# Optimization experiments

Measured on AMD Instinct MI355X. Metric: run time of the kernel, lower is better.

Reference implementation:

```python
import jax, jax.numpy as jnp
import numpy as np

B, H, S, D = 2, 16, 2048, 64

def setup_inputs() -> dict:
    key = jax.random.key(0)
    kq, kk, kv, km, ks = jax.random.split(key, 5)
    return {
        "query_input": jax.random.normal(kq, (B, H, S, D), dtype=jnp.float32),
        "key_input": jax.random.normal(kk, (B, H, S, D), dtype=jnp.float32),
        "value_input": jax.random.normal(kv, (B, H, S, D), dtype=jnp.float32),
        "query_mask": jnp.ones((B, 1, S, 1), dtype=jnp.float32),
        "key_mask": jax.random.uniform(km, (B, 1, 1, S), dtype=jnp.float32),
        "scale_factor": jax.random.normal(ks, (B, 1, 1, 1), dtype=jnp.float32),
        "dropout": 0,
    }

def reference(query_input, key_input, value_input, query_mask, key_mask, scale_factor, dropout):
    # qk = q @ k^T  -> [B, H, S, S]
    qk = jnp.einsum("bhqd,bhkd->bhqk", query_input, key_input)
    scaled_qk = qk * scale_factor                      # elementwise per-batch scale
    softmax_qk = jax.nn.softmax(scaled_qk, axis=-1)
    masked = softmax_qk * key_mask                     # post-softmax multiplicative mask
    # dropout with p=0 is the identity (deterministic baseline)
    output = jnp.einsum("bhqk,bhkd->bhqd", masked, value_input)
    return output
```

## Files before the change

kernel.cpp:

```cpp
#include <hip/hip_runtime.h>
#include <hip/hip_bf16.h>
#include <stdint.h>

#define BB 2
#define HH 16
#define SS 2048
#define DD 64
constexpr int BH = BB * HH;
constexpr int NT = SS / 64;
constexpr int QB = 16;

typedef _Float16 f16_t;
typedef f16_t f16x8 __attribute__((ext_vector_type(8)));
typedef float f32x4 __attribute__((ext_vector_type(4)));

__device__ __forceinline__ uint32_t pkf16(float a, float b) {
    return __builtin_bit_cast(uint32_t, __builtin_amdgcn_cvt_pkrtz(a, b));
}
__device__ __forceinline__ float fmax3(float a, float b, float c) {
    return fmaxf(fmaxf(a, b), c);
}

__global__ __launch_bounds__(256)
void prepack(const float* __restrict__ Kg, const float* __restrict__ Vg,
             const float* __restrict__ Mg, f16_t* __restrict__ Kp,
             f16_t* __restrict__ Vp)
{
    __shared__ float Vs[64][65];
    const int bh = blockIdx.x % BH;
    const int kt = blockIdx.x / BH;
    const int b  = bh / HH;
    const int t  = threadIdx.x;
    const size_t gbase = (size_t)bh * SS * DD + (size_t)kt * 64 * DD;
    const size_t tbase = ((size_t)bh * NT + kt) * 4096;

    for (int c = t; c < 512; c += 256) {
        const int row = c >> 3, j = c & 7;
        const float* kp = Kg + gbase + (size_t)row * DD + j * 8;
        float4 a = *(const float4*)kp;
        float4 d = *(const float4*)(kp + 4);
        uint4 w = make_uint4(pkf16(a.x, a.y), pkf16(a.z, a.w),
                             pkf16(d.x, d.y), pkf16(d.z, d.w));
        *(uint4*)&Kp[tbase + (size_t)row * 64 + ((j ^ (row & 7)) * 8)] = w;
    }

    for (int c = t; c < 1024; c += 256) {
        const int key = c >> 4, dc = (c & 15) * 4;
        float4 v = *(const float4*)(Vg + gbase + (size_t)key * DD + dc);
        const float m = Mg[(size_t)b * SS + kt * 64 + key];
        Vs[key][dc + 0] = v.x * m;
        Vs[key][dc + 1] = v.y * m;
        Vs[key][dc + 2] = v.z * m;
        Vs[key][dc + 3] = v.w * m;
    }
    __syncthreads();

    for (int c = t; c < 512; c += 256) {
        const int dr = c >> 3, j = c & 7;
        float v0 = Vs[j * 8 + 0][dr], v1 = Vs[j * 8 + 1][dr];
        float v2 = Vs[j * 8 + 2][dr], v3 = Vs[j * 8 + 3][dr];
        float v4 = Vs[j * 8 + 4][dr], v5 = Vs[j * 8 + 5][dr];
        float v6 = Vs[j * 8 + 6][dr], v7 = Vs[j * 8 + 7][dr];
        uint4 w = make_uint4(pkf16(v0, v1), pkf16(v2, v3),
                             pkf16(v4, v5), pkf16(v6, v7));
        *(uint4*)&Vp[tbase + (size_t)dr * 64 + ((j ^ (dr & 7)) * 8)] = w;
    }
}

__global__ __launch_bounds__(256)
void fattn12(const float* __restrict__ Qg, const f16_t* __restrict__ Kp,
             const f16_t* __restrict__ Vp, const float* __restrict__ Sg,
             float* __restrict__ Og)
{
    __shared__ __align__(16) f16_t Kt[2][4096];
    __shared__ __align__(16) f16_t Vt[3][4096];
    __shared__ __align__(16) f16_t Pt[4][2][16][72];

    const int bh   = blockIdx.x % BH;
    const int qt   = blockIdx.x / BH;
    const int b    = bh / HH;
    const int tid  = threadIdx.x;
    const int wave = tid >> 6;
    const int lane = tid & 63;
    const int l16  = lane & 15;
    const int quad = lane >> 4;

    const float sc = Sg[b] * 1.44269504088896340736f;
    const size_t base = (size_t)bh * SS * DD;
    const size_t tb0  = (size_t)bh * NT * 4096;
    const int q0 = qt * 128 + wave * 32;

    auto stage = [&](int kt, int kbuf, int vbuf) {
        const size_t toff = tb0 + (size_t)kt * 4096 + wave * 1024 + lane * 8;
        const f16_t* ks = Kp + toff;
        const f16_t* vs = Vp + toff;
        __builtin_amdgcn_global_load_lds(
            (const __attribute__((address_space(1))) void*)ks,
            (__attribute__((address_space(3))) void*)&Kt[kbuf][wave * 1024],
            16, 0, 0);
        __builtin_amdgcn_global_load_lds(
            (const __attribute__((address_space(1))) void*)(ks + 512),
            (__attribute__((address_space(3))) void*)&Kt[kbuf][wave * 1024 + 512],
            16, 0, 0);
        __builtin_amdgcn_global_load_lds(
            (const __attribute__((address_space(1))) void*)vs,
            (__attribute__((address_space(3))) void*)&Vt[vbuf][wave * 1024],
            16, 0, 0);
        __builtin_amdgcn_global_load_lds(
            (const __attribute__((address_space(1))) void*)(vs + 512),
            (__attribute__((address_space(3))) void*)&Vt[vbuf][wave * 1024 + 512],
            16, 0, 0);
    };

    stage(0, 0, 0);

    f16x8 qf[2][2];
#pragma unroll
    for (int g = 0; g < 2; ++g) {
        const float* qp = Qg + base + (size_t)(q0 + g * 16 + l16) * DD + quad * 8;
#pragma unroll
        for (int kc = 0; kc < 2; ++kc) {
            float4 a  = *(const float4*)(qp + kc * 32);
            float4 b4 = *(const float4*)(qp + kc * 32 + 4);
            f16x8 f;
            f[0] = (f16_t)(a.x * sc);  f[1] = (f16_t)(a.y * sc);
            f[2] = (f16_t)(a.z * sc);  f[3] = (f16_t)(a.w * sc);
            f[4] = (f16_t)(b4.x * sc); f[5] = (f16_t)(b4.y * sc);
            f[6] = (f16_t)(b4.z * sc); f[7] = (f16_t)(b4.w * sc);
            qf[g][kc] = f;
        }
    }

    f16x8 ones;
#pragma unroll
    for (int i = 0; i < 8; ++i) ones[i] = (f16_t)1.0f;

    f32x4 Ot[2][4];
#pragma unroll
    for (int g = 0; g < 2; ++g)
#pragma unroll
        for (int mt = 0; mt < 4; ++mt) Ot[g][mt] = f32x4{0.f, 0.f, 0.f, 0.f};
    f32x4 Osum[2] = {f32x4{0.f, 0.f, 0.f, 0.f}, f32x4{0.f, 0.f, 0.f, 0.f}};
    float m_run[2] = {-1e30f, -1e30f};

    const int swz = (l16 & 7) << 3;

    int vcur = 0;
    for (int kt = 0; kt < NT; ++kt) {
        const int kcur = kt & 1;
        const int vnxt = (vcur == 2) ? 0 : vcur + 1;
        if (kt + 1 < NT) {
            stage(kt + 1, kcur ^ 1, vnxt);
            asm volatile("s_waitcnt vmcnt(4)" ::: "memory");
        } else {
            asm volatile("s_waitcnt vmcnt(0)" ::: "memory");
        }
        __builtin_amdgcn_s_barrier();

        __builtin_amdgcn_s_setprio(1);
        f32x4 Sfr[2][4];
#pragma unroll
        for (int mt = 0; mt < 4; ++mt) {
            f32x4 a0 = f32x4{0.f, 0.f, 0.f, 0.f};
            f32x4 a1 = f32x4{0.f, 0.f, 0.f, 0.f};
#pragma unroll
            for (int kc = 0; kc < 2; ++kc) {
                const int off = (mt * 16 + l16) * 64 + ((kc * 32 + quad * 8) ^ swz);
                f16x8 kh = *(const f16x8*)&Kt[kcur][off];
                a0 = __builtin_amdgcn_mfma_f32_16x16x32_f16(kh, qf[0][kc], a0, 0, 0, 0);
                a1 = __builtin_amdgcn_mfma_f32_16x16x32_f16(kh, qf[1][kc], a1, 0, 0, 0);
            }
            Sfr[0][mt] = a0;
            Sfr[1][mt] = a1;
        }

        if (kt > 0) {
            const int vprv = (vcur == 0) ? 2 : vcur - 1;
#pragma unroll
            for (int kc = 0; kc < 2; ++kc) {
                f16x8 pf0 = *(const f16x8*)&Pt[wave][0][l16][kc * 32 + quad * 8];
                f16x8 pf1 = *(const f16x8*)&Pt[wave][1][l16][kc * 32 + quad * 8];
#pragma unroll
                for (int mt = 0; mt < 4; ++mt) {
                    const int off = (mt * 16 + l16) * 64 + ((kc * 32 + quad * 8) ^ swz);
                    f16x8 vf = *(const f16x8*)&Vt[vprv][off];
                    Ot[0][mt] = __builtin_amdgcn_mfma_f32_16x16x32_f16(vf, pf0, Ot[0][mt], 0, 0, 0);
                    Ot[1][mt] = __builtin_amdgcn_mfma_f32_16x16x32_f16(vf, pf1, Ot[1][mt], 0, 0, 0);
                }
                Osum[0] = __builtin_amdgcn_mfma_f32_16x16x32_f16(ones, pf0, Osum[0], 0, 0, 0);
                Osum[1] = __builtin_amdgcn_mfma_f32_16x16x32_f16(ones, pf1, Osum[1], 0, 0, 0);
            }
        }
        __builtin_amdgcn_s_setprio(0);

#pragma unroll
        for (int g = 0; g < 2; ++g) {
            float g0 = fmax3(Sfr[g][0][0], Sfr[g][0][1], Sfr[g][0][2]);
            float g1 = fmax3(Sfr[g][0][3], Sfr[g][1][0], Sfr[g][1][1]);
            float g2 = fmax3(Sfr[g][1][2], Sfr[g][1][3], Sfr[g][2][0]);
            float g3 = fmax3(Sfr[g][2][1], Sfr[g][2][2], Sfr[g][2][3]);
            float g4 = fmax3(Sfr[g][3][0], Sfr[g][3][1], Sfr[g][3][2]);
            float h0 = fmax3(g0, g1, Sfr[g][3][3]);
            float h1 = fmax3(g2, g3, g4);
            const float lmax = fmaxf(h0, h1);

            if (__any(lmax > m_run[g] + 8.0f)) {
                float mxq = fmaxf(lmax, __shfl_xor(lmax, 16));
                mxq = fmaxf(mxq, __shfl_xor(mxq, 32));
                const float mnew  = fmaxf(m_run[g], mxq);
                const float alpha = __builtin_amdgcn_exp2f(m_run[g] - mnew);
                m_run[g] = mnew;
#pragma unroll
                for (int mt = 0; mt < 4; ++mt) Ot[g][mt] *= alpha;
                Osum[g] *= alpha;
            }

            float ps[4][4];
#pragma unroll
            for (int mt = 0; mt < 4; ++mt)
#pragma unroll
                for (int r = 0; r < 4; ++r)
                    ps[mt][r] = __builtin_amdgcn_exp2f(Sfr[g][mt][r] - m_run[g]);

#pragma unroll
            for (int mt = 0; mt < 4; ++mt) {
                uint2 w = make_uint2(pkf16(ps[mt][0], ps[mt][1]),
                                     pkf16(ps[mt][2], ps[mt][3]));
                *(uint2*)&Pt[wave][g][l16][mt * 16 + quad * 4] = w;
            }
        }

        __builtin_amdgcn_s_barrier();
        vcur = vnxt;
    }

    {
        const int vprv = (vcur == 0) ? 2 : vcur - 1;
#pragma unroll
        for (int kc = 0; kc < 2; ++kc) {
            f16x8 pf0 = *(const f16x8*)&Pt[wave][0][l16][kc * 32 + quad * 8];
            f16x8 pf1 = *(const f16x8*)&Pt[wave][1][l16][kc * 32 + quad * 8];
#pragma unroll
            for (int mt = 0; mt < 4; ++mt) {
                const int off = (mt * 16 + l16) * 64 + ((kc * 32 + quad * 8) ^ swz);
                f16x8 vf = *(const f16x8*)&Vt[vprv][off];
                Ot[0][mt] = __builtin_amdgcn_mfma_f32_16x16x32_f16(vf, pf0, Ot[0][mt], 0, 0, 0);
                Ot[1][mt] = __builtin_amdgcn_mfma_f32_16x16x32_f16(vf, pf1, Ot[1][mt], 0, 0, 0);
            }
            Osum[0] = __builtin_amdgcn_mfma_f32_16x16x32_f16(ones, pf0, Osum[0], 0, 0, 0);
            Osum[1] = __builtin_amdgcn_mfma_f32_16x16x32_f16(ones, pf1, Osum[1], 0, 0, 0);
        }
    }

#pragma unroll
    for (int g = 0; g < 2; ++g) {
        const float inv = 1.0f / Osum[g][0];
        float* op = Og + base + (size_t)(q0 + g * 16 + l16) * DD + quad * 4;
#pragma unroll
        for (int mt = 0; mt < 4; ++mt) {
#pragma unroll
            for (int r = 0; r < 4; ++r)
                op[mt * 16 + r] = Ot[g][mt][r] * inv;
        }
    }
}

__global__ __launch_bounds__(512)
void fattn6(const float* __restrict__ Qg, const float* __restrict__ Kg,
            const float* __restrict__ Vg, const float* __restrict__ Mg,
            const float* __restrict__ Sg, float* __restrict__ Og)
{
    __shared__ __align__(16) f16_t Kh_lds[64][72];
    __shared__ __align__(16) f16_t Vt_lds[64][72];
    __shared__ __align__(16) f16_t Pt_lds[8][16][72];
    __shared__ float msk_lds[SS];

    const int bh   = blockIdx.x % BH;
    const int qt   = blockIdx.x / BH;
    const int b    = bh / HH;
    const int tid  = threadIdx.x;
    const int wave = tid >> 6;
    const int lane = tid & 63;
    const int l16  = lane & 15;
    const int quad = lane >> 4;

    const float sc = Sg[b] * 1.44269504088896340736f;
    const size_t base = (size_t)bh * SS * DD;
    const int q0 = qt * 128 + wave * 16;

    for (int i = tid; i < SS; i += 512) msk_lds[i] = Mg[(size_t)b * SS + i];

    f16x8 qf[2];
    {
        const float* qp = Qg + base + (size_t)(q0 + l16) * DD + quad * 8;
#pragma unroll
        for (int kc = 0; kc < 2; ++kc) {
            float4 a  = *(const float4*)(qp + kc * 32);
            float4 b4 = *(const float4*)(qp + kc * 32 + 4);
            f16x8 f;
            f[0] = (f16_t)(a.x * sc);  f[1] = (f16_t)(a.y * sc);
            f[2] = (f16_t)(a.z * sc);  f[3] = (f16_t)(a.w * sc);
            f[4] = (f16_t)(b4.x * sc); f[5] = (f16_t)(b4.y * sc);
            f[6] = (f16_t)(b4.z * sc); f[7] = (f16_t)(b4.w * sc);
            qf[kc] = f;
        }
    }

    f32x4 Ot[4];
#pragma unroll
    for (int mt = 0; mt < 4; ++mt) Ot[mt] = f32x4{0.f, 0.f, 0.f, 0.f};
    float m_run = -1e30f, l_run = 0.0f;

    const int krow = tid >> 3;
    const int kc8  = (tid & 7) * 8;
    const int vd   = tid & 63;
    const int vk0  = (tid >> 6) * 8;

    for (int kt = 0; kt < NT; ++kt) {
        __syncthreads();
        {
            const float* kp = Kg + base + (size_t)(kt * 64 + krow) * DD + kc8;
            float4 a0 = *(const float4*)(kp);
            float4 a1 = *(const float4*)(kp + 4);
            uint4 w = make_uint4(pkf16(a0.x, a0.y), pkf16(a0.z, a0.w),
                                 pkf16(a1.x, a1.y), pkf16(a1.z, a1.w));
            *(uint4*)&Kh_lds[krow][kc8] = w;
        }
        {
            const float* vp = Vg + base + (size_t)(kt * 64 + vk0) * DD + vd;
            const float* mp = &msk_lds[kt * 64 + vk0];
            float v0 = vp[0 * DD] * mp[0], v1 = vp[1 * DD] * mp[1];
            float v2 = vp[2 * DD] * mp[2], v3 = vp[3 * DD] * mp[3];
            float v4 = vp[4 * DD] * mp[4], v5 = vp[5 * DD] * mp[5];
            float v6 = vp[6 * DD] * mp[6], v7 = vp[7 * DD] * mp[7];
            uint4 w = make_uint4(pkf16(v0, v1), pkf16(v2, v3),
                                 pkf16(v4, v5), pkf16(v6, v7));
            *(uint4*)&Vt_lds[vd][vk0] = w;
        }
        __syncthreads();

        f32x4 Sfr[4];
#pragma unroll
        for (int mt = 0; mt < 4; ++mt) {
            f32x4 acc = f32x4{0.f, 0.f, 0.f, 0.f};
#pragma unroll
            for (int kc = 0; kc < 2; ++kc) {
                f16x8 kh = *(const f16x8*)&Kh_lds[mt * 16 + l16][kc * 32 + quad * 8];
                acc = __builtin_amdgcn_mfma_f32_16x16x32_f16(kh, qf[kc], acc, 0, 0, 0);
            }
            Sfr[mt] = acc;
        }

        float mx = Sfr[0][0];
#pragma unroll
        for (int mt = 0; mt < 4; ++mt)
#pragma unroll
            for (int r = 0; r < 4; ++r) mx = fmaxf(mx, Sfr[mt][r]);
        mx = fmaxf(mx, __shfl_xor(mx, 16));
        mx = fmaxf(mx, __shfl_xor(mx, 32));

        if (__any(mx > m_run)) {
            const float mnew  = fmaxf(m_run, mx);
            const float alpha = exp2f(m_run - mnew);
            m_run = mnew;
            l_run *= alpha;
#pragma unroll
            for (int mt = 0; mt < 4; ++mt) Ot[mt] *= alpha;
        }

        float ps[4][4];
        float rs = 0.0f;
#pragma unroll
        for (int mt = 0; mt < 4; ++mt)
#pragma unroll
            for (int r = 0; r < 4; ++r) {
                ps[mt][r] = exp2f(Sfr[mt][r] - m_run);
                rs += ps[mt][r];
            }
        rs += __shfl_xor(rs, 16);
        rs += __shfl_xor(rs, 32);
        l_run += rs;

#pragma unroll
        for (int mt = 0; mt < 4; ++mt) {
            uint2 w = make_uint2(pkf16(ps[mt][0], ps[mt][1]),
                                 pkf16(ps[mt][2], ps[mt][3]));
            *(uint2*)&Pt_lds[wave][l16][mt * 16 + quad * 4] = w;
        }

#pragma unroll
        for (int kc = 0; kc < 2; ++kc) {
            f16x8 pf = *(const f16x8*)&Pt_lds[wave][l16][kc * 32 + quad * 8];
#pragma unroll
            for (int mt = 0; mt < 4; ++mt) {
                f16x8 vf = *(const f16x8*)&Vt_lds[mt * 16 + l16][kc * 32 + quad * 8];
                Ot[mt] = __builtin_amdgcn_mfma_f32_16x16x32_f16(vf, pf, Ot[mt], 0, 0, 0);
            }
        }
    }

    const float inv = 1.0f / l_run;
    float* op = Og + base + (size_t)(q0 + l16) * DD + quad * 4;
#pragma unroll
    for (int mt = 0; mt < 4; ++mt) {
#pragma unroll
        for (int r = 0; r < 4; ++r)
            op[mt * 16 + r] = Ot[mt][r] * inv;
    }
}

extern "C" void kernel_launch(void* const* d_in, const int* in_sizes, int n_in,
                              void* d_out, int out_size, void* d_ws, size_t ws_size,
                              hipStream_t stream) {
    const float* Qg = (const float*)d_in[0];
    const float* Kg = (const float*)d_in[1];
    const float* Vg = (const float*)d_in[2];
    const float* Mg = (const float*)d_in[4];
    const float* Sg = (const float*)d_in[5];
    float* Og = (float*)d_out;

    const size_t kv_elems = (size_t)BH * SS * DD;
    const size_t need = 2 * kv_elems * sizeof(f16_t);

    if (d_ws != nullptr && ws_size >= need) {
        f16_t* Kp = (f16_t*)d_ws;
        f16_t* Vp = Kp + kv_elems;
        prepack<<<dim3(BH * NT), dim3(256), 0, stream>>>(Kg, Vg, Mg, Kp, Vp);
        fattn12<<<dim3(BH * QB), dim3(256), 0, stream>>>(Qg, Kp, Vp, Sg, Og);
    } else {
        fattn6<<<dim3(BH * QB), dim3(512), 0, stream>>>(Qg, Kg, Vg, Mg, Sg, Og);
    }
}
```

Baseline: 158.0 us.

## Shrink attention blocks to two waves and stage K ahead of V

Replaces the 4-wave, 128-query attention block with a 2-wave, 64-query block, doubling grid size to 1024 blocks with launch bounds allowing two blocks per SIMD. The pipeline is restructured: K for the next tile and V for the current tile are issued separately, V uses a double buffer instead of a triple buffer, and the loop is unrolled in pairs so buffer indices are compile-time constants. The aim is more blocks in flight, smaller shared memory per block, and cheaper buffer index arithmetic, at the cost of each block reloading K/V for fewer queries, so total K/V traffic doubles.

```diff
diff --git a/kernel.cpp b/kernel.cpp
--- a/kernel.cpp
+++ b/kernel.cpp
@@ -8,6 +8,7 @@
 #define DD 64
 constexpr int BH = BB * HH;
 constexpr int NT = SS / 64;
+constexpr int QB17 = 32;
 constexpr int QB = 16;
 
 typedef _Float16 f16_t;
@@ -67,14 +68,14 @@
     }
 }
 
-__global__ __launch_bounds__(256)
-void fattn12(const float* __restrict__ Qg, const f16_t* __restrict__ Kp,
+__global__ __launch_bounds__(128, 2)
+void fattn17(const float* __restrict__ Qg, const f16_t* __restrict__ Kp,
              const f16_t* __restrict__ Vp, const float* __restrict__ Sg,
              float* __restrict__ Og)
 {
     __shared__ __align__(16) f16_t Kt[2][4096];
-    __shared__ __align__(16) f16_t Vt[3][4096];
-    __shared__ __align__(16) f16_t Pt[4][2][16][72];
+    __shared__ __align__(16) f16_t Vt[2][4096];
+    __shared__ __align__(16) f16_t Pt[2][2][16][68];
 
     const int bh   = blockIdx.x % BH;
     const int qt   = blockIdx.x / BH;
@@ -88,31 +89,27 @@
     const float sc = Sg[b] * 1.44269504088896340736f;
     const size_t base = (size_t)bh * SS * DD;
     const size_t tb0  = (size_t)bh * NT * 4096;
-    const int q0 = qt * 128 + wave * 32;
-
-    auto stage = [&](int kt, int kbuf, int vbuf) {
-        const size_t toff = tb0 + (size_t)kt * 4096 + wave * 1024 + lane * 8;
-        const f16_t* ks = Kp + toff;
-        const f16_t* vs = Vp + toff;
-        __builtin_amdgcn_global_load_lds(
-            (const __attribute__((address_space(1))) void*)ks,
-            (__attribute__((address_space(3))) void*)&Kt[kbuf][wave * 1024],
-            16, 0, 0);
-        __builtin_amdgcn_global_load_lds(
-            (const __attribute__((address_space(1))) void*)(ks + 512),
-            (__attribute__((address_space(3))) void*)&Kt[kbuf][wave * 1024 + 512],
-            16, 0, 0);
-        __builtin_amdgcn_global_load_lds(
-            (const __attribute__((address_space(1))) void*)vs,
-            (__attribute__((address_space(3))) void*)&Vt[vbuf][wave * 1024],
-            16, 0, 0);
-        __builtin_amdgcn_global_load_lds(
-            (const __attribute__((address_space(1))) void*)(vs + 512),
-            (__attribute__((address_space(3))) void*)&Vt[vbuf][wave * 1024 + 512],
-            16, 0, 0);
+    const int q0 = qt * 64 + wave * 32;
+
+    const f16_t* kroot = Kp + tb0 + wave * 512 + lane * 8;
+    const f16_t* vroot = Vp + tb0 + wave * 512 + lane * 8;
+
+    auto stageK = [&](int t, int buf) {
+#pragma unroll
+        for (int i = 0; i < 4; ++i)
+            __builtin_amdgcn_global_load_lds(
+                (const __attribute__((address_space(1))) void*)(kroot + (size_t)t * 4096 + i * 1024),
+                (__attribute__((address_space(3))) void*)&Kt[buf][i * 1024 + wave * 512], 16, 0, 0);
     };
-
-    stage(0, 0, 0);
+    auto stageV = [&](int t, int buf) {
+#pragma unroll
+        for (int i = 0; i < 4; ++i)
+            __builtin_amdgcn_global_load_lds(
+                (const __attribute__((address_space(1))) void*)(vroot + (size_t)t * 4096 + i * 1024),
+                (__attribute__((address_space(3))) void*)&Vt[buf][i * 1024 + wave * 512], 16, 0, 0);
+    };
+
+    stageK(0, 0);
 
     f16x8 qf[2][2];
 #pragma unroll
@@ -145,16 +142,11 @@
 
     const int swz = (l16 & 7) << 3;
 
-    int vcur = 0;
-    for (int kt = 0; kt < NT; ++kt) {
-        const int kcur = kt & 1;
-        const int vnxt = (vcur == 2) ? 0 : vcur + 1;
-        if (kt + 1 < NT) {
-            stage(kt + 1, kcur ^ 1, vnxt);
-            asm volatile("s_waitcnt vmcnt(4)" ::: "memory");
-        } else {
-            asm volatile("s_waitcnt vmcnt(0)" ::: "memory");
-        }
+    auto phase = [&](int t, int ksb, int vsb, int krb, int vrb, bool doPV) {
+        const int tk = (t + 1 < NT) ? (t + 1) : (NT - 1);
+        stageK(tk, ksb);
+        stageV(t, vsb);
+        asm volatile("s_waitcnt vmcnt(8)" ::: "memory");
         __builtin_amdgcn_s_barrier();
 
         __builtin_amdgcn_s_setprio(1);
@@ -166,7 +158,7 @@
 #pragma unroll
             for (int kc = 0; kc < 2; ++kc) {
                 const int off = (mt * 16 + l16) * 64 + ((kc * 32 + quad * 8) ^ swz);
-                f16x8 kh = *(const f16x8*)&Kt[kcur][off];
+                f16x8 kh = *(const f16x8*)&Kt[krb][off];
                 a0 = __builtin_amdgcn_mfma_f32_16x16x32_f16(kh, qf[0][kc], a0, 0, 0, 0);
                 a1 = __builtin_amdgcn_mfma_f32_16x16x32_f16(kh, qf[1][kc], a1, 0, 0, 0);
             }
@@ -174,8 +166,7 @@
             Sfr[1][mt] = a1;
         }
 
-        if (kt > 0) {
-            const int vprv = (vcur == 0) ? 2 : vcur - 1;
+        if (doPV) {
 #pragma unroll
             for (int kc = 0; kc < 2; ++kc) {
                 f16x8 pf0 = *(const f16x8*)&Pt[wave][0][l16][kc * 32 + quad * 8];
@@ -183,7 +174,7 @@
 #pragma unroll
                 for (int mt = 0; mt < 4; ++mt) {
                     const int off = (mt * 16 + l16) * 64 + ((kc * 32 + quad * 8) ^ swz);
-                    f16x8 vf = *(const f16x8*)&Vt[vprv][off];
+                    f16x8 vf = *(const f16x8*)&Vt[vrb][off];
                     Ot[0][mt] = __builtin_amdgcn_mfma_f32_16x16x32_f16(vf, pf0, Ot[0][mt], 0, 0, 0);
                     Ot[1][mt] = __builtin_amdgcn_mfma_f32_16x16x32_f16(vf, pf1, Ot[1][mt], 0, 0, 0);
                 }
@@ -231,11 +222,18 @@
         }
 
         __builtin_amdgcn_s_barrier();
-        vcur = vnxt;
-    }
-
+    };
+
+    phase(0, 1, 0, 0, 1, false);
+    phase(1, 0, 1, 1, 0, true);
+    for (int j = 1; j < NT / 2; ++j) {
+        phase(2 * j,     1, 0, 0, 1, true);
+        phase(2 * j + 1, 0, 1, 1, 0, true);
+    }
+
+    asm volatile("s_waitcnt vmcnt(0)" ::: "memory");
+    __builtin_amdgcn_s_barrier();
     {
-        const int vprv = (vcur == 0) ? 2 : vcur - 1;
 #pragma unroll
         for (int kc = 0; kc < 2; ++kc) {
             f16x8 pf0 = *(const f16x8*)&Pt[wave][0][l16][kc * 32 + quad * 8];
@@ -243,7 +241,7 @@
 #pragma unroll
             for (int mt = 0; mt < 4; ++mt) {
                 const int off = (mt * 16 + l16) * 64 + ((kc * 32 + quad * 8) ^ swz);
-                f16x8 vf = *(const f16x8*)&Vt[vprv][off];
+                f16x8 vf = *(const f16x8*)&Vt[1][off];
                 Ot[0][mt] = __builtin_amdgcn_mfma_f32_16x16x32_f16(vf, pf0, Ot[0][mt], 0, 0, 0);
                 Ot[1][mt] = __builtin_amdgcn_mfma_f32_16x16x32_f16(vf, pf1, Ot[1][mt], 0, 0, 0);
             }
@@ -426,7 +424,7 @@
         f16_t* Kp = (f16_t*)d_ws;
         f16_t* Vp = Kp + kv_elems;
         prepack<<<dim3(BH * NT), dim3(256), 0, stream>>>(Kg, Vg, Mg, Kp, Vp);
-        fattn12<<<dim3(BH * QB), dim3(256), 0, stream>>>(Qg, Kp, Vp, Sg, Og);
+        fattn17<<<dim3(BH * QB17), dim3(128), 0, stream>>>(Qg, Kp, Vp, Sg, Og);
     } else {
         fattn6<<<dim3(BH * QB), dim3(512), 0, stream>>>(Qg, Kg, Vg, Mg, Sg, Og);
     }
```

After: 176.6 us. 11.8% more time.
